# Optimization experiments

Hardware: AMD Instinct MI355X
Metric: run time of the kernel (lower is better)

The kernel has to match this reference:

```python
import jax, jax.numpy as jnp
import numpy as np

LN_EPS = 1e-5

def setup_inputs() -> dict:
    key = jax.random.key(0)
    B, S, D = 4, 2048, 1024
    ks = jax.random.split(key, 8)
    sc = 1.0 / np.sqrt(D)
    inp = {
        'x': jax.random.normal(ks[0], (B, S, D), jnp.float32),
        'Wq': jax.random.normal(ks[1], (D, D), jnp.float32) * sc,
        'bq': jnp.zeros((D,), jnp.float32),
        'Wk': jax.random.normal(ks[2], (D, D), jnp.float32) * sc,
        'bk': jnp.zeros((D,), jnp.float32),
        'Wv': jax.random.normal(ks[3], (D, D), jnp.float32) * sc,
        'bv': jnp.zeros((D,), jnp.float32),
        'Wo': jax.random.normal(ks[4], (D, D), jnp.float32) * sc,
        'bo': jnp.zeros((D,), jnp.float32),
        'Wg_val': jax.random.normal(ks[5], (D, D), jnp.float32) * sc,
        'bg_val': jnp.zeros((D,), jnp.float32),
        'Wg_gate': jax.random.normal(ks[6], (D, D), jnp.float32) * sc,
        'bg_gate': jnp.zeros((D,), jnp.float32),
        'gamma': jnp.ones((D,), jnp.float32),
        'beta': jnp.zeros((D,), jnp.float32),
    }
    return inp


def reference(x, Wq, bq, Wk, bk, Wv, bv, Wo, bo, Wg_val, bg_val, Wg_gate, bg_gate, gamma, beta):
    # x: [B,S,D]
    q = jnp.einsum('bsd,de->bse', x, Wq) + bq
    k = jnp.einsum('bsd,de->bse', x, Wk) + bk
    v = jnp.einsum('bsd,de->bse', x, Wv) + bv
    scale = 1.0 / jnp.sqrt(jnp.asarray(q.shape[-1], q.dtype))
    qk = jnp.einsum('bqe,bke->bqk', q, k) * scale  # [B,S,S]
    a = jax.nn.softmax(qk, axis=-1)
    out = jnp.einsum('bqk,bke->bqe', a, v)
    out = jnp.einsum('bse,ed->bsd', out, Wo) + bo
    # GLU residual on q, then LayerNorm
    glu = (jnp.einsum('bse,ed->bsd', q, Wg_val) + bg_val) * jax.nn.sigmoid(jnp.einsum('bse,ed->bsd', q, Wg_gate) + bg_gate)
    out = out + glu
    mu = jnp.mean(out, axis=-1, keepdims=True)
    var = jnp.var(out, axis=-1, keepdims=True)
    out = (out - mu) * jax.lax.rsqrt(var + LN_EPS) * gamma + beta
    return out
```

## Files before the change

### kernel.cpp

```cpp
#include <hip/hip_runtime.h>
#include <hip/hip_bf16.h>
#include <cstdint>


typedef __bf16 bf16x8 __attribute__((ext_vector_type(8)));
typedef __bf16 bf16x4 __attribute__((ext_vector_type(4)));
typedef float f32x4 __attribute__((ext_vector_type(4)));

#define SYNC() do { asm volatile("" ::: "memory"); __builtin_amdgcn_s_barrier(); asm volatile("" ::: "memory"); } while (0)
#define WAITV(n) asm volatile("s_waitcnt vmcnt(" #n ")" ::: "memory")

__device__ __forceinline__ void gload_lds16(const void* g, void* l) {
    __builtin_amdgcn_global_load_lds(
        (__attribute__((address_space(1))) void*)(uintptr_t)g,
        (__attribute__((address_space(3))) void*)(uintptr_t)l,
        16, 0, 0);
}

template <int EPI>
__global__ __launch_bounds__(512, 1) void gemm256(
    const __hip_bfloat16* __restrict__ A1, int lda1,
    const __hip_bfloat16* __restrict__ A2, int lda2, int nsplit,
    const __hip_bfloat16* __restrict__ Bt,
    __hip_bfloat16* __restrict__ Cout, const float* __restrict__ bias, float scale,
    int K, int ldb, int ldc,
    long strideA, long strideB, long strideC)
{
    __shared__ __align__(16) char smem[131072];

    const int b = blockIdx.z;
    const int tid = threadIdx.x;
    const int lane = tid & 63;
    const int wm = (tid >> 6) & 1;
    const int wn = (tid >> 6) >> 1;

    const bool sel2 = ((int)blockIdx.y * 256) >= nsplit;
    const __hip_bfloat16* A = sel2 ? A2 : A1;
    const int lda = sel2 ? lda2 : lda1;

    const __hip_bfloat16* gA = A + (long)b * strideA + (long)blockIdx.x * 256 * lda;
    const __hip_bfloat16* gB = Bt + (long)b * strideB + (long)blockIdx.y * 256 * ldb;

    const int r0 = tid >> 3;
    const int s0 = (tid & 7) ^ (r0 & 7);
    const int r1 = r0 + 64;
    const int s1 = (tid & 7) ^ (r1 & 7);

#define STAGE(buf, isB, half, kt)                                                        \
    do {                                                                                 \
        const __hip_bfloat16* g_ = (isB) ? gB : gA;                                      \
        const int ld_ = (isB) ? ldb : lda;                                               \
        char* l_ = smem + (buf) * 65536 + (isB) * 32768 + (half) * 16384;                \
        gload_lds16(g_ + (long)((half) * 128 + r0) * ld_ + (kt) * 64 + s0 * 8, l_ + tid * 16);        \
        gload_lds16(g_ + (long)((half) * 128 + r1) * ld_ + (kt) * 64 + s1 * 8, l_ + 8192 + tid * 16); \
    } while (0)

    const int fr = lane & 15;
    const int kg = lane >> 4;

#define LDA_(dst, buf, mh, mi, kk)                                                       \
    do {                                                                                 \
        const int lr_ = wm * 64 + (mi) * 16 + fr;                                        \
        const int sl_ = ((kk) * 4 + kg) ^ (lr_ & 7);                                     \
        dst = *(const bf16x8*)(smem + (buf) * 65536 + (mh) * 16384 + lr_ * 128 + sl_ * 16); \
    } while (0)
#define LDB_(dst, buf, nh, ni, kk)                                                       \
    do {                                                                                 \
        const int lr_ = wn * 32 + (ni) * 16 + fr;                                        \
        const int sl_ = ((kk) * 4 + kg) ^ (lr_ & 7);                                     \
        dst = *(const bf16x8*)(smem + (buf) * 65536 + 32768 + (nh) * 16384 + lr_ * 128 + sl_ * 16); \
    } while (0)

    f32x4 acc[2][2][4][2];
#pragma unroll
    for (int mh = 0; mh < 2; ++mh)
#pragma unroll
        for (int nh = 0; nh < 2; ++nh)
#pragma unroll
            for (int mi = 0; mi < 4; ++mi)
#pragma unroll
                for (int ni = 0; ni < 2; ++ni) acc[mh][nh][mi][ni] = {0.f, 0.f, 0.f, 0.f};

    bf16x8 av[4][2], bv[2][2];

#define MFMA_QUAD(mh, nh)                                                                \
    do {                                                                                 \
        __builtin_amdgcn_s_setprio(1);                                                   \
        _Pragma("unroll")                                                                \
        for (int mi = 0; mi < 4; ++mi)                                                   \
            _Pragma("unroll")                                                            \
            for (int ni = 0; ni < 2; ++ni)                                               \
                _Pragma("unroll")                                                        \
                for (int kk = 0; kk < 2; ++kk)                                           \
                    acc[mh][nh][mi][ni] = __builtin_amdgcn_mfma_f32_16x16x32_bf16(       \
                        av[mi][kk], bv[ni][kk], acc[mh][nh][mi][ni], 0, 0, 0);           \
        __builtin_amdgcn_s_setprio(0);                                                   \
    } while (0)

    const int NT = K >> 6;

    STAGE(0, 0, 0, 0);
    STAGE(0, 1, 0, 0);
    STAGE(0, 1, 1, 0);
    STAGE(0, 0, 1, 0);
    WAITV(4);
    SYNC();

    for (int t = 0; t < NT - 1; ++t) {
        const int c = t & 1;
#pragma unroll
        for (int mi = 0; mi < 4; ++mi) { LDA_(av[mi][0], c, 0, mi, 0); LDA_(av[mi][1], c, 0, mi, 1); }
#pragma unroll
        for (int ni = 0; ni < 2; ++ni) { LDB_(bv[ni][0], c, 0, ni, 0); LDB_(bv[ni][1], c, 0, ni, 1); }
        STAGE(c ^ 1, 0, 0, t + 1);
        MFMA_QUAD(0, 0);
        WAITV(4);
        SYNC();
#pragma unroll
        for (int ni = 0; ni < 2; ++ni) { LDB_(bv[ni][0], c, 1, ni, 0); LDB_(bv[ni][1], c, 1, ni, 1); }
        STAGE(c ^ 1, 1, 0, t + 1);
        MFMA_QUAD(0, 1);
        WAITV(4);
        SYNC();
#pragma unroll
        for (int mi = 0; mi < 4; ++mi) { LDA_(av[mi][0], c, 1, mi, 0); LDA_(av[mi][1], c, 1, mi, 1); }
        STAGE(c ^ 1, 1, 1, t + 1);
        MFMA_QUAD(1, 1);
        SYNC();
#pragma unroll
        for (int ni = 0; ni < 2; ++ni) { LDB_(bv[ni][0], c, 0, ni, 0); LDB_(bv[ni][1], c, 0, ni, 1); }
        STAGE(c ^ 1, 0, 1, t + 1);
        MFMA_QUAD(1, 0);
        WAITV(4);
        SYNC();
    }

    {
        const int c = (NT - 1) & 1;
#pragma unroll
        for (int mi = 0; mi < 4; ++mi) { LDA_(av[mi][0], c, 0, mi, 0); LDA_(av[mi][1], c, 0, mi, 1); }
#pragma unroll
        for (int ni = 0; ni < 2; ++ni) { LDB_(bv[ni][0], c, 0, ni, 0); LDB_(bv[ni][1], c, 0, ni, 1); }
        MFMA_QUAD(0, 0);
        WAITV(2);
        SYNC();
#pragma unroll
        for (int ni = 0; ni < 2; ++ni) { LDB_(bv[ni][0], c, 1, ni, 0); LDB_(bv[ni][1], c, 1, ni, 1); }
        MFMA_QUAD(0, 1);
        WAITV(0);
        SYNC();
#pragma unroll
        for (int mi = 0; mi < 4; ++mi) { LDA_(av[mi][0], c, 1, mi, 0); LDA_(av[mi][1], c, 1, mi, 1); }
        MFMA_QUAD(1, 1);
#pragma unroll
        for (int ni = 0; ni < 2; ++ni) { LDB_(bv[ni][0], c, 0, ni, 0); LDB_(bv[ni][1], c, 0, ni, 1); }
        MFMA_QUAD(1, 0);
    }

    const long row0 = (long)blockIdx.x * 256 + wm * 64 + (lane >> 4) * 4;
    const long col0 = (long)blockIdx.y * 256 + wn * 32 + (lane & 15);
#pragma unroll
    for (int mh = 0; mh < 2; ++mh) {
#pragma unroll
        for (int nh = 0; nh < 2; ++nh) {
#pragma unroll
            for (int ni = 0; ni < 2; ++ni) {
                const long col = col0 + nh * 128 + ni * 16;
                const float bval = (EPI == 0 && bias != nullptr) ? bias[col] : 0.f;
#pragma unroll
                for (int mi = 0; mi < 4; ++mi) {
                    const long row = row0 + mh * 128 + mi * 16;
#pragma unroll
                    for (int i = 0; i < 4; ++i) {
                        const float v = (EPI == 1) ? acc[mh][nh][mi][ni][i] * scale
                                                   : acc[mh][nh][mi][ni][i] + bval;
                        Cout[(long)b * strideC + (row + i) * (long)ldc + col] = __float2bfloat16(v);
                    }
                }
            }
        }
    }
#undef STAGE
#undef LDA_
#undef LDB_
#undef MFMA_QUAD
}

template <int VOUT>
__global__ __launch_bounds__(512, 1) void gemm_tn128(
    const __hip_bfloat16* __restrict__ A, int lda,
    const __hip_bfloat16* __restrict__ Bt,
    __hip_bfloat16* __restrict__ Cout, const float* __restrict__ bias,
    __hip_bfloat16* __restrict__ vt,
    int K, int ldb, int ldc,
    long strideA, long strideB, long strideC)
{
    __shared__ __align__(16) char smem[147456];

    const int b = blockIdx.z;
    const int tid = threadIdx.x;
    const int lane = tid & 63;
    const int wid = tid >> 6;
    const int wm = wid & 3;
    const int wn = wid >> 2;

    const __hip_bfloat16* gA = A + (long)b * strideA + (long)blockIdx.x * 256 * lda;
    const __hip_bfloat16* gB = Bt + (long)b * strideB + (long)blockIdx.y * 128 * ldb;

    const int r0 = tid >> 3, r1 = r0 + 64;
    const int s0 = (tid & 7) ^ (r0 & 7);
    const int s1 = (tid & 7) ^ (r1 & 7);

#define STG_A(base_, h_, kt_)                                                                              \
    do {                                                                                                   \
        gload_lds16(gA + (long)((h_) * 128 + r0) * lda + (kt_) * 64 + s0 * 8, (base_) + (h_) * 16384 + tid * 16);        \
        gload_lds16(gA + (long)((h_) * 128 + r1) * lda + (kt_) * 64 + s1 * 8, (base_) + (h_) * 16384 + 8192 + tid * 16); \
    } while (0)
#define STG_B(base_, kt_)                                                                                  \
    do {                                                                                                   \
        gload_lds16(gB + (long)r0 * ldb + (kt_) * 64 + s0 * 8, (base_) + 32768 + tid * 16);                \
        gload_lds16(gB + (long)r1 * ldb + (kt_) * 64 + s1 * 8, (base_) + 32768 + 8192 + tid * 16);         \
    } while (0)

    const int fr = lane & 15;
    const int kg = lane >> 4;

#define LD_A(dst, base_, mi_, kk_)                                                        \
    do {                                                                                  \
        const int row_ = wm * 64 + (mi_) * 16 + fr;                                       \
        const int sl_ = ((kk_) * 4 + kg) ^ (row_ & 7);                                    \
        dst = *(const bf16x8*)((base_) + row_ * 128 + sl_ * 16);                          \
    } while (0)
#define LD_B(dst, base_, ni_, kk_)                                                        \
    do {                                                                                  \
        const int row_ = wn * 64 + (ni_) * 16 + fr;                                       \
        const int sl_ = ((kk_) * 4 + kg) ^ (row_ & 7);                                    \
        dst = *(const bf16x8*)((base_) + 32768 + row_ * 128 + sl_ * 16);                  \
    } while (0)

    f32x4 acc[4][4];
#pragma unroll
    for (int mi = 0; mi < 4; ++mi)
#pragma unroll
        for (int ni = 0; ni < 4; ++ni) acc[mi][ni] = {0.f, 0.f, 0.f, 0.f};

    const int NT = K >> 6;

    STG_A(smem, 0, 0); STG_A(smem, 1, 0); STG_B(smem, 0);
    STG_A(smem + 49152, 0, 1); STG_A(smem + 49152, 1, 1); STG_B(smem + 49152, 1);
    WAITV(6);
    SYNC();

    int bi = 0;
    for (int t = 0; t < NT; ++t) {
        char* base = smem + bi * 49152;
        if (t + 2 < NT) {
            int bs = bi + 2; if (bs >= 3) bs -= 3;
            char* sb = smem + bs * 49152;
            STG_A(sb, 0, t + 2); STG_A(sb, 1, t + 2); STG_B(sb, t + 2);
        }
        bf16x8 av[4], bv[4];
#pragma unroll
        for (int kk = 0; kk < 2; ++kk) {
#pragma unroll
            for (int mi = 0; mi < 4; ++mi) LD_A(av[mi], base, mi, kk);
#pragma unroll
            for (int ni = 0; ni < 4; ++ni) LD_B(bv[ni], base, ni, kk);
            __builtin_amdgcn_s_setprio(1);
#pragma unroll
            for (int mi = 0; mi < 4; ++mi)
#pragma unroll
                for (int ni = 0; ni < 4; ++ni)
                    acc[mi][ni] = __builtin_amdgcn_mfma_f32_16x16x32_bf16(av[mi], bv[ni], acc[mi][ni], 0, 0, 0);
            __builtin_amdgcn_s_setprio(0);
        }
        if (t + 2 < NT) { WAITV(6); SYNC(); }
        else if (t + 1 < NT) { WAITV(0); SYNC(); }
        bi = (bi + 1 == 3) ? 0 : bi + 1;
    }

    const long row0 = (long)blockIdx.x * 256 + wm * 64 + (lane >> 4) * 4;
    const long col0 = (long)blockIdx.y * 128 + wn * 64 + (lane & 15);
    if (VOUT) {
#pragma unroll
        for (int mi = 0; mi < 4; ++mi) {
#pragma unroll
            for (int i = 0; i < 4; ++i) {
                const long row = row0 + mi * 16 + i;
                const float bval = (bias != nullptr) ? bias[row] : 0.f;
#pragma unroll
                for (int ni = 0; ni < 4; ++ni) {
                    const long col = col0 + ni * 16;
                    const long vb = col >> 11;
                    const long vs = col & 2047;
                    vt[(vb << 21) + row * 2048 + vs] = __float2bfloat16(acc[mi][ni][i] + bval);
                }
            }
        }
    } else {
#pragma unroll
        for (int ni = 0; ni < 4; ++ni) {
            const long col = col0 + ni * 16;
            const float bval = (bias != nullptr) ? bias[col] : 0.f;
#pragma unroll
            for (int mi = 0; mi < 4; ++mi) {
                const long row = row0 + mi * 16;
#pragma unroll
                for (int i = 0; i < 4; ++i)
                    Cout[(long)b * strideC + (row + i) * (long)ldc + col] = __float2bfloat16(acc[mi][ni][i] + bval);
            }
        }
    }
#undef STG_A
#undef STG_B
#undef LD_A
#undef LD_B
}

__global__ __launch_bounds__(256) void transpose6(
    const float* __restrict__ W0, const float* __restrict__ W1, const float* __restrict__ W2,
    const float* __restrict__ W3, const float* __restrict__ W4, const float* __restrict__ W5,
    __hip_bfloat16* __restrict__ dst)
{
    __shared__ float tile[32][33];
    const int z = blockIdx.z;
    const float* pin = (z == 0) ? W0 : (z == 1) ? W1 : (z == 2) ? W2 : (z == 3) ? W3 : (z == 4) ? W4 : W5;
    __hip_bfloat16* pout = dst + (long)z * 1024 * 1024;
    const int tx = threadIdx.x, ty = threadIdx.y;
    const int c0 = blockIdx.x * 32, r0 = blockIdx.y * 32;
#pragma unroll
    for (int j = 0; j < 4; ++j)
        tile[ty + j * 8][tx] = pin[(long)(r0 + ty + j * 8) * 1024 + c0 + tx];
    __syncthreads();
#pragma unroll
    for (int j = 0; j < 4; ++j)
        pout[(long)(c0 + ty + j * 8) * 1024 + r0 + tx] = __float2bfloat16(tile[tx][ty + j * 8]);
}

__global__ __launch_bounds__(256) void f32_to_bf16_vec(
    const float* __restrict__ in, __hip_bfloat16* __restrict__ out, long n4)
{
    const long i = (long)blockIdx.x * 256 + threadIdx.x;
    if (i >= n4) return;
    const float4 v = ((const float4*)in)[i];
    union { __hip_bfloat16 h[4]; ushort4 u; } cv;
    cv.h[0] = __float2bfloat16(v.x);
    cv.h[1] = __float2bfloat16(v.y);
    cv.h[2] = __float2bfloat16(v.z);
    cv.h[3] = __float2bfloat16(v.w);
    ((ushort4*)out)[i] = cv.u;
}

__global__ __launch_bounds__(256) void concat_bias(
    const float* __restrict__ bq, const float* __restrict__ bk, const float* __restrict__ bv,
    const float* __restrict__ bo, const float* __restrict__ bgv, const float* __restrict__ bgg,
    float* __restrict__ out)
{
    const int i = blockIdx.x * 256 + threadIdx.x;
    float v;
    if (i < 1024) v = bq[i];
    else if (i < 2048) v = bk[i - 1024];
    else if (i < 3072) v = bv[i - 2048];
    else if (i < 4096) v = bo[i - 3072];
    else if (i < 5120) v = bgv[i - 4096];
    else v = bgg[i - 5120];
    out[i] = v;
}

__global__ __launch_bounds__(256) void softmax_kernel(
    const __hip_bfloat16* __restrict__ S, __hip_bfloat16* __restrict__ P)
{
    const long row = blockIdx.x;
    const __hip_bfloat16* s = S + row * 2048;
    __hip_bfloat16* p = P + row * 2048;
    const int t = threadIdx.x;
    const bf16x8 v8 = *(const bf16x8*)(s + t * 8);
    float v[8];
    float mx = -1e30f;
#pragma unroll
    for (int j = 0; j < 8; ++j) { v[j] = (float)v8[j]; mx = fmaxf(mx, v[j]); }
#pragma unroll
    for (int off = 32; off; off >>= 1) mx = fmaxf(mx, __shfl_xor(mx, off));
    __shared__ float wred[4];
    __shared__ float wsum[4];
    const int w = t >> 6;
    if ((t & 63) == 0) wred[w] = mx;
    __syncthreads();
    mx = fmaxf(fmaxf(wred[0], wred[1]), fmaxf(wred[2], wred[3]));
    float sum = 0.f;
#pragma unroll
    for (int j = 0; j < 8; ++j) { v[j] = __expf(v[j] - mx); sum += v[j]; }
#pragma unroll
    for (int off = 32; off; off >>= 1) sum += __shfl_xor(sum, off);
    if ((t & 63) == 0) wsum[w] = sum;
    __syncthreads();
    sum = wsum[0] + wsum[1] + wsum[2] + wsum[3];
    const float inv = 1.0f / sum;
    bf16x8 o8;
#pragma unroll
    for (int j = 0; j < 8; ++j) o8[j] = (__bf16)(v[j] * inv);
    *(bf16x8*)(p + t * 8) = o8;
}

__global__ __launch_bounds__(256) void glu_ln_kernel(
    const __hip_bfloat16* __restrict__ T1G,
    const float* __restrict__ gamma, const float* __restrict__ beta, float* __restrict__ out)
{
    const long row = blockIdx.x;
    const __hip_bfloat16* pr = T1G + row * 3072;
    const int t = threadIdx.x;
    const int c0 = t * 4;
    const bf16x4 t1 = *(const bf16x4*)(pr + c0);
    const bf16x4 gv = *(const bf16x4*)(pr + 1024 + c0);
    const bf16x4 gg = *(const bf16x4*)(pr + 2048 + c0);
    float y[4];
    float s = 0.f, ss = 0.f;
#pragma unroll
    for (int j = 0; j < 4; ++j) {
        const float g = (float)gv[j] * (1.0f / (1.0f + __expf(-(float)gg[j])));
        const float val = (float)t1[j] + g;
        y[j] = val; s += val; ss += val * val;
    }
#pragma unroll
    for (int off = 32; off; off >>= 1) { s += __shfl_xor(s, off); ss += __shfl_xor(ss, off); }
    __shared__ float rs[4], rss[4];
    const int w = t >> 6;
    if ((t & 63) == 0) { rs[w] = s; rss[w] = ss; }
    __syncthreads();
    s = rs[0] + rs[1] + rs[2] + rs[3];
    ss = rss[0] + rss[1] + rss[2] + rss[3];
    const float mu = s * (1.0f / 1024.0f);
    const float var = ss * (1.0f / 1024.0f) - mu * mu;
    const float r = rsqrtf(var + 1e-5f);
    const float4 gm = *(const float4*)(gamma + c0);
    const float4 bt = *(const float4*)(beta + c0);
    float4 o;
    o.x = (y[0] - mu) * r * gm.x + bt.x;
    o.y = (y[1] - mu) * r * gm.y + bt.y;
    o.z = (y[2] - mu) * r * gm.z + bt.z;
    o.w = (y[3] - mu) * r * gm.w + bt.w;
    *(float4*)(out + row * 1024 + c0) = o;
}

extern "C" void kernel_launch(void* const* d_in, const int* in_sizes, int n_in,
                              void* d_out, int out_size, void* d_ws, size_t ws_size,
                              hipStream_t stream)
{
    const int B = 4, S = 2048, D = 1024;
    const float* x    = (const float*)d_in[0];
    const float* Wq   = (const float*)d_in[1];
    const float* bq   = (const float*)d_in[2];
    const float* Wk   = (const float*)d_in[3];
    const float* bk   = (const float*)d_in[4];
    const float* Wv   = (const float*)d_in[5];
    const float* bv   = (const float*)d_in[6];
    const float* Wo   = (const float*)d_in[7];
    const float* bo   = (const float*)d_in[8];
    const float* Wgv  = (const float*)d_in[9];
    const float* bgv  = (const float*)d_in[10];
    const float* Wgg  = (const float*)d_in[11];
    const float* bgg  = (const float*)d_in[12];
    const float* gamma = (const float*)d_in[13];
    const float* beta  = (const float*)d_in[14];
    float* out = (float*)d_out;

    char* ws = (char*)d_ws;
    size_t off = 0;
    auto take = [&](size_t bytes) { char* p = ws + off; off += (bytes + 255) & ~(size_t)255; return p; };

    __hip_bfloat16* wcat   = (__hip_bfloat16*)take((size_t)6 * D * D * 2);
    float*          bcat   = (float*)take((size_t)6 * D * 4);
    __hip_bfloat16* xb     = (__hip_bfloat16*)take((size_t)B * S * D * 2);
    __hip_bfloat16* QKb    = (__hip_bfloat16*)take((size_t)B * S * 2 * D * 2);
    __hip_bfloat16* Vtb    = (__hip_bfloat16*)take((size_t)B * S * D * 2);
    __hip_bfloat16* scoresb = (__hip_bfloat16*)take((size_t)B * S * S * 2);
    __hip_bfloat16* Pb     = (__hip_bfloat16*)take((size_t)B * S * S * 2);
    __hip_bfloat16* Oatt   = (__hip_bfloat16*)take((size_t)B * S * D * 2);
    __hip_bfloat16* T1G    = (__hip_bfloat16*)take((size_t)B * S * 3 * D * 2);

    const long SD = (long)S * D, SS = (long)S * S, S2D = (long)S * 2 * D;
    const float att_scale = 0.03125f;
    const __hip_bfloat16* Qb = QKb;
    const __hip_bfloat16* Kb = QKb + D;

    f32_to_bf16_vec<<<dim3((unsigned)((long)B * S * D / 4 / 256)), dim3(256), 0, stream>>>(x, xb, (long)B * S * D / 4);
    transpose6<<<dim3(D / 32, D / 32, 6), dim3(32, 8), 0, stream>>>(Wq, Wk, Wv, Wo, Wgv, Wgg, wcat);
    concat_bias<<<dim3(24), dim3(256), 0, stream>>>(bq, bk, bv, bo, bgv, bgg, bcat);

    gemm256<0><<<dim3(B * S / 256, 2 * D / 256, 1), dim3(512), 0, stream>>>(
        xb, D, xb, D, 1 << 30, wcat, QKb, bcat, 1.f,
        D, D, 2 * D, 0, 0, 0);

    gemm_tn128<1><<<dim3(D / 256, B * S / 128, 1), dim3(512), 0, stream>>>(
        wcat + (size_t)2 * D * D, D, xb, nullptr, bcat + 2 * D, Vtb,
        D, D, 0, 0, 0, 0);

    gemm256<1><<<dim3(S / 256, S / 256, B), dim3(512), 0, stream>>>(
        Qb, 2 * D, Qb, 2 * D, 1 << 30, Kb, scoresb, nullptr, att_scale,
        D, 2 * D, S, S2D, S2D, SS);

    softmax_kernel<<<dim3(B * S), dim3(256), 0, stream>>>(scoresb, Pb);

    gemm_tn128<0><<<dim3(S / 256, D / 128, B), dim3(512), 0, stream>>>(
        Pb, S, Vtb, Oatt, nullptr, nullptr, S, S, D, SS, SD, SD);

    gemm256<0><<<dim3(B * S / 256, 2 * D / 256, 1), dim3(512), 0, stream>>>(
        Oatt, D, QKb, 2 * D, D, wcat + (size_t)3 * D * D, T1G, bcat + 3 * D, 1.f,
        D, D, 3 * D, 0, 0, 0);

    gemm_tn128<0><<<dim3(B * S / 256, D / 128, 1), dim3(512), 0, stream>>>(
        QKb, 2 * D, wcat + (size_t)5 * D * D, T1G + 2 * D, bcat + 5 * D, nullptr,
        D, D, 3 * D, 0, 0, 0);

    glu_ln_kernel<<<dim3(B * S), dim3(256), 0, stream>>>(T1G, gamma, beta, out);
}
```

Baseline: 239.9 us.

## Merge V-transpose GEMM and GLU-gate GEMM into one 256-tile dual kernel

Adds a gemm256_dual kernel whose first 128 blocks compute the transposed V projection and whose remaining 128 blocks compute the GLU gate projection (q times Wg_gate), both on the 256x256 pipelined tile body. That body is pulled out into shared macros so both kernels can use it. Two separate 128-wide tile launches are replaced by one launch of 256 blocks, which cuts launch count and improves CU fill and per-tile reuse. In exchange, the gate GEMM now runs before the attention GEMMs, and the V-transposed scatter store is kept with its strided writes.

```diff
diff --git a/kernel.cpp b/kernel.cpp
--- a/kernel.cpp
+++ b/kernel.cpp
@@ -16,6 +16,97 @@
         (__attribute__((address_space(3))) void*)(uintptr_t)l,
         16, 0, 0);
 }
+
+#define STAGE(buf, isB, half, kt)                                                        \
+    do {                                                                                 \
+        const __hip_bfloat16* g_ = (isB) ? gB : gA;                                      \
+        const int ld_ = (isB) ? ldb : lda;                                               \
+        char* l_ = smem + (buf) * 65536 + (isB) * 32768 + (half) * 16384;                \
+        gload_lds16(g_ + (long)((half) * 128 + r0) * ld_ + (kt) * 64 + s0 * 8, l_ + tid * 16);        \
+        gload_lds16(g_ + (long)((half) * 128 + r1) * ld_ + (kt) * 64 + s1 * 8, l_ + 8192 + tid * 16); \
+    } while (0)
+#define LDA_(dst, buf, mh, mi, kk)                                                       \
+    do {                                                                                 \
+        const int lr_ = wm * 64 + (mi) * 16 + fr;                                        \
+        const int sl_ = ((kk) * 4 + kg) ^ (lr_ & 7);                                     \
+        dst = *(const bf16x8*)(smem + (buf) * 65536 + (mh) * 16384 + lr_ * 128 + sl_ * 16); \
+    } while (0)
+#define LDB_(dst, buf, nh, ni, kk)                                                       \
+    do {                                                                                 \
+        const int lr_ = wn * 32 + (ni) * 16 + fr;                                        \
+        const int sl_ = ((kk) * 4 + kg) ^ (lr_ & 7);                                     \
+        dst = *(const bf16x8*)(smem + (buf) * 65536 + 32768 + (nh) * 16384 + lr_ * 128 + sl_ * 16); \
+    } while (0)
+#define MFMA_QUAD(mh, nh)                                                                \
+    do {                                                                                 \
+        __builtin_amdgcn_s_setprio(1);                                                   \
+        _Pragma("unroll")                                                                \
+        for (int mi = 0; mi < 4; ++mi)                                                   \
+            _Pragma("unroll")                                                            \
+            for (int ni = 0; ni < 2; ++ni)                                               \
+                _Pragma("unroll")                                                        \
+                for (int kk = 0; kk < 2; ++kk)                                           \
+                    acc[mh][nh][mi][ni] = __builtin_amdgcn_mfma_f32_16x16x32_bf16(       \
+                        av[mi][kk], bv[ni][kk], acc[mh][nh][mi][ni], 0, 0, 0);           \
+        __builtin_amdgcn_s_setprio(0);                                                   \
+    } while (0)
+
+#define GEMM256_BODY(NT)                                                                 \
+    STAGE(0, 0, 0, 0);                                                                   \
+    STAGE(0, 1, 0, 0);                                                                   \
+    STAGE(0, 1, 1, 0);                                                                   \
+    STAGE(0, 0, 1, 0);                                                                   \
+    WAITV(4);                                                                            \
+    SYNC();                                                                              \
+    for (int t = 0; t < (NT) - 1; ++t) {                                                 \
+        const int c = t & 1;                                                             \
+        _Pragma("unroll")                                                                \
+        for (int mi = 0; mi < 4; ++mi) { LDA_(av[mi][0], c, 0, mi, 0); LDA_(av[mi][1], c, 0, mi, 1); } \
+        _Pragma("unroll")                                                                \
+        for (int ni = 0; ni < 2; ++ni) { LDB_(bv[ni][0], c, 0, ni, 0); LDB_(bv[ni][1], c, 0, ni, 1); } \
+        STAGE(c ^ 1, 0, 0, t + 1);                                                       \
+        MFMA_QUAD(0, 0);                                                                 \
+        WAITV(4);                                                                        \
+        SYNC();                                                                          \
+        _Pragma("unroll")                                                                \
+        for (int ni = 0; ni < 2; ++ni) { LDB_(bv[ni][0], c, 1, ni, 0); LDB_(bv[ni][1], c, 1, ni, 1); } \
+        STAGE(c ^ 1, 1, 0, t + 1);                                                       \
+        MFMA_QUAD(0, 1);                                                                 \
+        WAITV(4);                                                                        \
+        SYNC();                                                                          \
+        _Pragma("unroll")                                                                \
+        for (int mi = 0; mi < 4; ++mi) { LDA_(av[mi][0], c, 1, mi, 0); LDA_(av[mi][1], c, 1, mi, 1); } \
+        STAGE(c ^ 1, 1, 1, t + 1);                                                       \
+        MFMA_QUAD(1, 1);                                                                 \
+        SYNC();                                                                          \
+        _Pragma("unroll")                                                                \
+        for (int ni = 0; ni < 2; ++ni) { LDB_(bv[ni][0], c, 0, ni, 0); LDB_(bv[ni][1], c, 0, ni, 1); } \
+        STAGE(c ^ 1, 0, 1, t + 1);                                                       \
+        MFMA_QUAD(1, 0);                                                                 \
+        WAITV(4);                                                                        \
+        SYNC();                                                                          \
+    }                                                                                    \
+    {                                                                                    \
+        const int c = ((NT) - 1) & 1;                                                    \
+        _Pragma("unroll")                                                                \
+        for (int mi = 0; mi < 4; ++mi) { LDA_(av[mi][0], c, 0, mi, 0); LDA_(av[mi][1], c, 0, mi, 1); } \
+        _Pragma("unroll")                                                                \
+        for (int ni = 0; ni < 2; ++ni) { LDB_(bv[ni][0], c, 0, ni, 0); LDB_(bv[ni][1], c, 0, ni, 1); } \
+        MFMA_QUAD(0, 0);                                                                 \
+        WAITV(2);                                                                        \
+        SYNC();                                                                          \
+        _Pragma("unroll")                                                                \
+        for (int ni = 0; ni < 2; ++ni) { LDB_(bv[ni][0], c, 1, ni, 0); LDB_(bv[ni][1], c, 1, ni, 1); } \
+        MFMA_QUAD(0, 1);                                                                 \
+        WAITV(0);                                                                        \
+        SYNC();                                                                          \
+        _Pragma("unroll")                                                                \
+        for (int mi = 0; mi < 4; ++mi) { LDA_(av[mi][0], c, 1, mi, 0); LDA_(av[mi][1], c, 1, mi, 1); } \
+        MFMA_QUAD(1, 1);                                                                 \
+        _Pragma("unroll")                                                                \
+        for (int ni = 0; ni < 2; ++ni) { LDB_(bv[ni][0], c, 0, ni, 0); LDB_(bv[ni][1], c, 0, ni, 1); } \
+        MFMA_QUAD(1, 0);                                                                 \
+    }
 
 template <int EPI>
 __global__ __launch_bounds__(512, 1) void gemm256(
@@ -45,32 +136,9 @@
     const int s0 = (tid & 7) ^ (r0 & 7);
     const int r1 = r0 + 64;
     const int s1 = (tid & 7) ^ (r1 & 7);
-
-#define STAGE(buf, isB, half, kt)                                                        \
-    do {                                                                                 \
-        const __hip_bfloat16* g_ = (isB) ? gB : gA;                                      \
-        const int ld_ = (isB) ? ldb : lda;                                               \
-        char* l_ = smem + (buf) * 65536 + (isB) * 32768 + (half) * 16384;                \
-        gload_lds16(g_ + (long)((half) * 128 + r0) * ld_ + (kt) * 64 + s0 * 8, l_ + tid * 16);        \
-        gload_lds16(g_ + (long)((half) * 128 + r1) * ld_ + (kt) * 64 + s1 * 8, l_ + 8192 + tid * 16); \
-    } while (0)
-
     const int fr = lane & 15;
     const int kg = lane >> 4;
 
-#define LDA_(dst, buf, mh, mi, kk)                                                       \
-    do {                                                                                 \
-        const int lr_ = wm * 64 + (mi) * 16 + fr;                                        \
-        const int sl_ = ((kk) * 4 + kg) ^ (lr_ & 7);                                     \
-        dst = *(const bf16x8*)(smem + (buf) * 65536 + (mh) * 16384 + lr_ * 128 + sl_ * 16); \
-    } while (0)
-#define LDB_(dst, buf, nh, ni, kk)                                                       \
-    do {                                                                                 \
-        const int lr_ = wn * 32 + (ni) * 16 + fr;                                        \
-        const int sl_ = ((kk) * 4 + kg) ^ (lr_ & 7);                                     \
-        dst = *(const bf16x8*)(smem + (buf) * 65536 + 32768 + (nh) * 16384 + lr_ * 128 + sl_ * 16); \
-    } while (0)
-
     f32x4 acc[2][2][4][2];
 #pragma unroll
     for (int mh = 0; mh < 2; ++mh)
@@ -80,82 +148,10 @@
             for (int mi = 0; mi < 4; ++mi)
 #pragma unroll
                 for (int ni = 0; ni < 2; ++ni) acc[mh][nh][mi][ni] = {0.f, 0.f, 0.f, 0.f};
-
     bf16x8 av[4][2], bv[2][2];
 
-#define MFMA_QUAD(mh, nh)                                                                \
-    do {                                                                                 \
-        __builtin_amdgcn_s_setprio(1);                                                   \
-        _Pragma("unroll")                                                                \
-        for (int mi = 0; mi < 4; ++mi)                                                   \
-            _Pragma("unroll")                                                            \
-            for (int ni = 0; ni < 2; ++ni)                                               \
-                _Pragma("unroll")                                                        \
-                for (int kk = 0; kk < 2; ++kk)                                           \
-                    acc[mh][nh][mi][ni] = __builtin_amdgcn_mfma_f32_16x16x32_bf16(       \
-                        av[mi][kk], bv[ni][kk], acc[mh][nh][mi][ni], 0, 0, 0);           \
-        __builtin_amdgcn_s_setprio(0);                                                   \
-    } while (0)
-
     const int NT = K >> 6;
-
-    STAGE(0, 0, 0, 0);
-    STAGE(0, 1, 0, 0);
-    STAGE(0, 1, 1, 0);
-    STAGE(0, 0, 1, 0);
-    WAITV(4);
-    SYNC();
-
-    for (int t = 0; t < NT - 1; ++t) {
-        const int c = t & 1;
-#pragma unroll
-        for (int mi = 0; mi < 4; ++mi) { LDA_(av[mi][0], c, 0, mi, 0); LDA_(av[mi][1], c, 0, mi, 1); }
-#pragma unroll
-        for (int ni = 0; ni < 2; ++ni) { LDB_(bv[ni][0], c, 0, ni, 0); LDB_(bv[ni][1], c, 0, ni, 1); }
-        STAGE(c ^ 1, 0, 0, t + 1);
-        MFMA_QUAD(0, 0);
-        WAITV(4);
-        SYNC();
-#pragma unroll
-        for (int ni = 0; ni < 2; ++ni) { LDB_(bv[ni][0], c, 1, ni, 0); LDB_(bv[ni][1], c, 1, ni, 1); }
-        STAGE(c ^ 1, 1, 0, t + 1);
-        MFMA_QUAD(0, 1);
-        WAITV(4);
-        SYNC();
-#pragma unroll
-        for (int mi = 0; mi < 4; ++mi) { LDA_(av[mi][0], c, 1, mi, 0); LDA_(av[mi][1], c, 1, mi, 1); }
-        STAGE(c ^ 1, 1, 1, t + 1);
-        MFMA_QUAD(1, 1);
-        SYNC();
-#pragma unroll
-        for (int ni = 0; ni < 2; ++ni) { LDB_(bv[ni][0], c, 0, ni, 0); LDB_(bv[ni][1], c, 0, ni, 1); }
-        STAGE(c ^ 1, 0, 1, t + 1);
-        MFMA_QUAD(1, 0);
-        WAITV(4);
-        SYNC();
-    }
-
-    {
-        const int c = (NT - 1) & 1;
-#pragma unroll
-        for (int mi = 0; mi < 4; ++mi) { LDA_(av[mi][0], c, 0, mi, 0); LDA_(av[mi][1], c, 0, mi, 1); }
-#pragma unroll
-        for (int ni = 0; ni < 2; ++ni) { LDB_(bv[ni][0], c, 0, ni, 0); LDB_(bv[ni][1], c, 0, ni, 1); }
-        MFMA_QUAD(0, 0);
-        WAITV(2);
-        SYNC();
-#pragma unroll
-        for (int ni = 0; ni < 2; ++ni) { LDB_(bv[ni][0], c, 1, ni, 0); LDB_(bv[ni][1], c, 1, ni, 1); }
-        MFMA_QUAD(0, 1);
-        WAITV(0);
-        SYNC();
-#pragma unroll
-        for (int mi = 0; mi < 4; ++mi) { LDA_(av[mi][0], c, 1, mi, 0); LDA_(av[mi][1], c, 1, mi, 1); }
-        MFMA_QUAD(1, 1);
-#pragma unroll
-        for (int ni = 0; ni < 2; ++ni) { LDB_(bv[ni][0], c, 0, ni, 0); LDB_(bv[ni][1], c, 0, ni, 1); }
-        MFMA_QUAD(1, 0);
-    }
+    GEMM256_BODY(NT)
 
     const long row0 = (long)blockIdx.x * 256 + wm * 64 + (lane >> 4) * 4;
     const long col0 = (long)blockIdx.y * 256 + wn * 32 + (lane & 15);
@@ -180,18 +176,102 @@
             }
         }
     }
-#undef STAGE
-#undef LDA_
-#undef LDB_
-#undef MFMA_QUAD
-}
-
-template <int VOUT>
+}
+
+__global__ __launch_bounds__(512, 1) void gemm256_dual(
+    const __hip_bfloat16* __restrict__ wvT,
+    const __hip_bfloat16* __restrict__ xb,
+    const __hip_bfloat16* __restrict__ Qp,
+    const __hip_bfloat16* __restrict__ wggT,
+    __hip_bfloat16* __restrict__ vt,
+    __hip_bfloat16* __restrict__ T1G,
+    const float* __restrict__ bv,
+    const float* __restrict__ bgg)
+{
+    __shared__ __align__(16) char smem[131072];
+
+    const int bid = blockIdx.x;
+    const bool isVt = bid < 128;
+    const int tid = threadIdx.x;
+    const int lane = tid & 63;
+    const int wm = (tid >> 6) & 1;
+    const int wn = (tid >> 6) >> 1;
+
+    int mx, my, lda, ldb;
+    const __hip_bfloat16 *Aop, *Bop;
+    if (isVt) { mx = bid >> 5; my = bid & 31; Aop = wvT; lda = 1024; Bop = xb;   ldb = 1024; }
+    else { const int t2 = bid - 128; mx = t2 >> 2; my = t2 & 3; Aop = Qp; lda = 2048; Bop = wggT; ldb = 1024; }
+
+    const __hip_bfloat16* gA = Aop + (long)mx * 256 * lda;
+    const __hip_bfloat16* gB = Bop + (long)my * 256 * ldb;
+
+    const int r0 = tid >> 3;
+    const int s0 = (tid & 7) ^ (r0 & 7);
+    const int r1 = r0 + 64;
+    const int s1 = (tid & 7) ^ (r1 & 7);
+    const int fr = lane & 15;
+    const int kg = lane >> 4;
+
+    f32x4 acc[2][2][4][2];
+#pragma unroll
+    for (int mh = 0; mh < 2; ++mh)
+#pragma unroll
+        for (int nh = 0; nh < 2; ++nh)
+#pragma unroll
+            for (int mi = 0; mi < 4; ++mi)
+#pragma unroll
+                for (int ni = 0; ni < 2; ++ni) acc[mh][nh][mi][ni] = {0.f, 0.f, 0.f, 0.f};
+    bf16x8 av[4][2], bv2[2][2];
+    #define bv bv2
+    GEMM256_BODY(16)
+    #undef bv
+
+    const long row0 = (long)mx * 256 + wm * 64 + (lane >> 4) * 4;
+    const long col0 = (long)my * 256 + wn * 32 + (lane & 15);
+    if (isVt) {
+#pragma unroll
+        for (int mh = 0; mh < 2; ++mh)
+#pragma unroll
+            for (int nh = 0; nh < 2; ++nh)
+#pragma unroll
+                for (int ni = 0; ni < 2; ++ni) {
+                    const long col = col0 + nh * 128 + ni * 16;
+                    const long vb = col >> 11, vs = col & 2047;
+#pragma unroll
+                    for (int mi = 0; mi < 4; ++mi) {
+#pragma unroll
+                        for (int i = 0; i < 4; ++i) {
+                            const long row = row0 + mh * 128 + mi * 16 + i;
+                            vt[(vb << 21) + row * 2048 + vs] =
+                                __float2bfloat16(acc[mh][nh][mi][ni][i] + bv[row]);
+                        }
+                    }
+                }
+    } else {
+#pragma unroll
+        for (int mh = 0; mh < 2; ++mh)
+#pragma unroll
+            for (int nh = 0; nh < 2; ++nh)
+#pragma unroll
+                for (int ni = 0; ni < 2; ++ni) {
+                    const long col = col0 + nh * 128 + ni * 16;
+                    const float bval = bgg[col];
+#pragma unroll
+                    for (int mi = 0; mi < 4; ++mi) {
+                        const long row = row0 + mh * 128 + mi * 16;
+#pragma unroll
+                        for (int i = 0; i < 4; ++i)
+                            T1G[(row + i) * 3072 + 2048 + col] =
+                                __float2bfloat16(acc[mh][nh][mi][ni][i] + bval);
+                    }
+                }
+    }
+}
+
 __global__ __launch_bounds__(512, 1) void gemm_tn128(
     const __hip_bfloat16* __restrict__ A, int lda,
     const __hip_bfloat16* __restrict__ Bt,
     __hip_bfloat16* __restrict__ Cout, const float* __restrict__ bias,
-    __hip_bfloat16* __restrict__ vt,
     int K, int ldb, int ldc,
     long strideA, long strideB, long strideC)
 {
@@ -259,19 +339,19 @@
             char* sb = smem + bs * 49152;
             STG_A(sb, 0, t + 2); STG_A(sb, 1, t + 2); STG_B(sb, t + 2);
         }
-        bf16x8 av[4], bv[4];
+        bf16x8 av[4], bvv[4];
 #pragma unroll
         for (int kk = 0; kk < 2; ++kk) {
 #pragma unroll
             for (int mi = 0; mi < 4; ++mi) LD_A(av[mi], base, mi, kk);
 #pragma unroll
-            for (int ni = 0; ni < 4; ++ni) LD_B(bv[ni], base, ni, kk);
+            for (int ni = 0; ni < 4; ++ni) LD_B(bvv[ni], base, ni, kk);
             __builtin_amdgcn_s_setprio(1);
 #pragma unroll
             for (int mi = 0; mi < 4; ++mi)
 #pragma unroll
                 for (int ni = 0; ni < 4; ++ni)
-                    acc[mi][ni] = __builtin_amdgcn_mfma_f32_16x16x32_bf16(av[mi], bv[ni], acc[mi][ni], 0, 0, 0);
+                    acc[mi][ni] = __builtin_amdgcn_mfma_f32_16x16x32_bf16(av[mi], bvv[ni], acc[mi][ni], 0, 0, 0);
             __builtin_amdgcn_s_setprio(0);
         }
         if (t + 2 < NT) { WAITV(6); SYNC(); }
@@ -281,34 +361,16 @@
 
     const long row0 = (long)blockIdx.x * 256 + wm * 64 + (lane >> 4) * 4;
     const long col0 = (long)blockIdx.y * 128 + wn * 64 + (lane & 15);
-    if (VOUT) {
+#pragma unroll
+    for (int ni = 0; ni < 4; ++ni) {
+        const long col = col0 + ni * 16;
+        const float bval = (bias != nullptr) ? bias[col] : 0.f;
 #pragma unroll
         for (int mi = 0; mi < 4; ++mi) {
-#pragma unroll
-            for (int i = 0; i < 4; ++i) {
-                const long row = row0 + mi * 16 + i;
-                const float bval = (bias != nullptr) ? bias[row] : 0.f;
-#pragma unroll
-                for (int ni = 0; ni < 4; ++ni) {
-                    const long col = col0 + ni * 16;
-                    const long vb = col >> 11;
-                    const long vs = col & 2047;
-                    vt[(vb << 21) + row * 2048 + vs] = __float2bfloat16(acc[mi][ni][i] + bval);
-                }
-            }
-        }
-    } else {
-#pragma unroll
-        for (int ni = 0; ni < 4; ++ni) {
-            const long col = col0 + ni * 16;
-            const float bval = (bias != nullptr) ? bias[col] : 0.f;
-#pragma unroll
-            for (int mi = 0; mi < 4; ++mi) {
-                const long row = row0 + mi * 16;
-#pragma unroll
-                for (int i = 0; i < 4; ++i)
-                    Cout[(long)b * strideC + (row + i) * (long)ldc + col] = __float2bfloat16(acc[mi][ni][i] + bval);
-            }
+            const long row = row0 + mi * 16;
+#pragma unroll
+            for (int i = 0; i < 4; ++i)
+                Cout[(long)b * strideC + (row + i) * (long)ldc + col] = __float2bfloat16(acc[mi][ni][i] + bval);
         }
     }
 #undef STG_A
@@ -491,9 +553,9 @@
         xb, D, xb, D, 1 << 30, wcat, QKb, bcat, 1.f,
         D, D, 2 * D, 0, 0, 0);
 
-    gemm_tn128<1><<<dim3(D / 256, B * S / 128, 1), dim3(512), 0, stream>>>(
-        wcat + (size_t)2 * D * D, D, xb, nullptr, bcat + 2 * D, Vtb,
-        D, D, 0, 0, 0, 0);
+    gemm256_dual<<<dim3(256), dim3(512), 0, stream>>>(
+        wcat + (size_t)2 * D * D, xb, QKb, wcat + (size_t)5 * D * D,
+        Vtb, T1G, bcat + 2 * D, bcat + 5 * D);
 
     gemm256<1><<<dim3(S / 256, S / 256, B), dim3(512), 0, stream>>>(
         Qb, 2 * D, Qb, 2 * D, 1 << 30, Kb, scoresb, nullptr, att_scale,
@@ -501,16 +563,12 @@
 
     softmax_kernel<<<dim3(B * S), dim3(256), 0, stream>>>(scoresb, Pb);
 
-    gemm_tn128<0><<<dim3(S / 256, D / 128, B), dim3(512), 0, stream>>>(
-        Pb, S, Vtb, Oatt, nullptr, nullptr, S, S, D, SS, SD, SD);
+    gemm_tn128<<<dim3(S / 256, D / 128, B), dim3(512), 0, stream>>>(
+        Pb, S, Vtb, Oatt, nullptr, S, S, D, SS, SD, SD);
 
     gemm256<0><<<dim3(B * S / 256, 2 * D / 256, 1), dim3(512), 0, stream>>>(
         Oatt, D, QKb, 2 * D, D, wcat + (size_t)3 * D * D, T1G, bcat + 3 * D, 1.f,
         D, D, 3 * D, 0, 0, 0);
 
-    gemm_tn128<0><<<dim3(B * S / 256, D / 128, 1), dim3(512), 0, stream>>>(
-        QKb, 2 * D, wcat + (size_t)5 * D * D, T1G + 2 * D, bcat + 5 * D, nullptr,
-        D, D, 3 * D, 0, 0, 0);
-
     glu_ln_kernel<<<dim3(B * S), dim3(256), 0, stream>>>(T1G, gamma, beta, out);
 }
```

Result: faster. 226.0 us (-5.8%).
